# Optimization experiments

Measured on AMD Instinct MI355X. Metric: run time of the kernel, lower is better.

The kernel has to match this reference:

```python
import jax, jax.numpy as jnp
import numpy as np

E = 16      # num experts
K = 2       # top-k
EPS = np.finfo(float).eps


def setup_inputs() -> dict:
    key = jax.random.key(0)
    k1, k2, k3 = jax.random.split(key, 3)
    B, D_IN, D_OUT = 16384, 1024, 512
    x = jax.random.normal(k1, (B, D_IN), dtype=jnp.float32)
    w_router = jax.random.normal(k2, (D_IN, E), dtype=jnp.float32) * 0.02
    w_experts = jax.random.normal(k3, (E, D_IN, D_OUT), dtype=jnp.float32) * 0.02
    return {"x": x, "w_router": w_router, "w_experts": w_experts}


def reference(x, w_router, w_experts):
    # --- noisy_top_k_gating (eval path: clean logits, no noise) ---
    logits = x @ w_router                      # [B, E]
    top_vals, top_idx = jax.lax.top_k(logits, K)   # [B, K]
    top_gates = jax.nn.softmax(top_vals, axis=1)   # softmax over top-k logits
    B = x.shape[0]
    gates = jnp.zeros_like(logits).at[jnp.arange(B)[:, None], top_idx].set(top_gates)  # [B, E]

    # --- per-expert encode (dense form; zero gates null out non-dispatched pairs,
    #     matching SparseDispatcher's sparse dispatch/combine math exactly) ---
    expert_out = jnp.einsum('bd,edh->beh', x, w_experts)  # [B, E, d_out]

    # --- SparseDispatcher.combine: exp -> gate-weight -> index_add -> eps clamp -> log ---
    combined = jnp.einsum('be,beh->bh', gates, jnp.exp(expert_out))  # [B, d_out]
    combined = jnp.where(combined == 0, jnp.asarray(EPS, combined.dtype), combined)
    return jnp.log(combined)
```

## Files before the change

kernel.cpp:

```cpp
#include <hip/hip_runtime.h>
#include <hip/hip_bf16.h>

typedef unsigned short u16_t;
typedef unsigned int   u32_t;

#define B_ROWS  16384
#define D_IN    1024
#define D_OUT   512
#define NEXP    16
#define CNT_STRIDE 16
#define EPSF    2.2204460492503131e-16f

using short8  = __attribute__((ext_vector_type(8))) short;
using floatx4 = __attribute__((ext_vector_type(4))) float;

__device__ __forceinline__ u16_t f2bf(float f) {
    u32_t u = __float_as_uint(f);
    u += 0x7fffu + ((u >> 16) & 1u);
    return (u16_t)(u >> 16);
}

__global__ __launch_bounds__(256) void prep_kernel(
        const float* __restrict__ x, const float* __restrict__ wr,
        const float* __restrict__ we,
        u16_t* __restrict__ xb, float* __restrict__ wrT,
        u16_t* __restrict__ wT, int* __restrict__ counts) {
    __shared__ u16_t sh[128][72];
    int blk = blockIdx.x;
    int t = threadIdx.x;
    if (blk < 8192) {
        if (blk == 0) counts[t] = 0;
        size_t i = ((size_t)blk * 256 + t) * 8;
        float4 a = *(const float4*)(x + i);
        float4 b = *(const float4*)(x + i + 4);
        union { u16_t us[8]; uint4 v; } p;
        p.us[0] = f2bf(a.x); p.us[1] = f2bf(a.y); p.us[2] = f2bf(a.z); p.us[3] = f2bf(a.w);
        p.us[4] = f2bf(b.x); p.us[5] = f2bf(b.y); p.us[6] = f2bf(b.z); p.us[7] = f2bf(b.w);
        *(uint4*)(xb + i) = p.v;
    } else if (blk < 9216) {
        int b = blk - 8192;
        int e = b >> 6, k0 = ((b >> 3) & 7) * 128, n0 = (b & 7) * 64;
        int kk = t >> 4, nc = (t & 15) * 4;
        const float* src = we + ((size_t)e * D_IN + k0 + kk) * D_OUT + n0 + nc;
        #pragma unroll
        for (int p = 0; p < 8; ++p) {
            float4 v = *(const float4*)(src + (size_t)p * 16 * D_OUT);
            sh[p * 16 + kk][nc + 0] = f2bf(v.x);
            sh[p * 16 + kk][nc + 1] = f2bf(v.y);
            sh[p * 16 + kk][nc + 2] = f2bf(v.z);
            sh[p * 16 + kk][nc + 3] = f2bf(v.w);
        }
        __syncthreads();
        int nn = t >> 2, c = t & 3;
        u16_t* dst = wT + ((size_t)e * D_OUT + n0 + nn) * D_IN + k0 + c * 32;
        #pragma unroll
        for (int j = 0; j < 4; ++j) {
            union { u16_t us[8]; uint4 v; } p;
            #pragma unroll
            for (int jj = 0; jj < 8; ++jj) p.us[jj] = sh[c * 32 + j * 8 + jj][nn];
            *(uint4*)(dst + j * 8) = p.v;
        }
    } else {
        int i = (blk - 9216) * 256 + t;
        int e = i >> 10, d = i & 1023;
        wrT[i] = wr[d * NEXP + e];
    }
}

__global__ __launch_bounds__(256) void router_kernel(
        const float* __restrict__ x, const float* __restrict__ wrT,
        int* __restrict__ counts, int* __restrict__ rowlist,
        float* __restrict__ gatelist) {
    __shared__ float wsh[NEXP * D_IN];
    __shared__ int hist[NEXP], base[NEXP], hist2[NEXP];
    __shared__ unsigned char eidx_sh[32][2];
    __shared__ float g_sh[32][2];

    int t = threadIdx.x;
    {
        const float4* src = (const float4*)wrT;
        float4* dst = (float4*)wsh;
        #pragma unroll
        for (int i = 0; i < 16; ++i) dst[t + 256 * i] = src[t + 256 * i];
    }
    if (t < NEXP) { hist[t] = 0; hist2[t] = 0; }
    __syncthreads();

    int lr = t >> 3, q = t & 7;
    int row = blockIdx.x * 32 + lr;
    const float4* xq = (const float4*)(x + (size_t)row * D_IN);

    double acc[NEXP];
    #pragma unroll
    for (int e = 0; e < NEXP; ++e) acc[e] = 0.0;

    for (int i = 0; i < 32; ++i) {
        float4 xv = xq[i * 8 + q];
        double x0 = xv.x, x1 = xv.y, x2 = xv.z, x3 = xv.w;
        #pragma unroll
        for (int e = 0; e < NEXP; ++e) {
            float4 wv = *(const float4*)(&wsh[e * D_IN + i * 32 + q * 4]);
            acc[e] += x0 * (double)wv.x;
            acc[e] += x1 * (double)wv.y;
            acc[e] += x2 * (double)wv.z;
            acc[e] += x3 * (double)wv.w;
        }
    }
    #pragma unroll
    for (int e = 0; e < NEXP; ++e) {
        acc[e] += __shfl_xor(acc[e], 1);
        acc[e] += __shfl_xor(acc[e], 2);
        acc[e] += __shfl_xor(acc[e], 4);
    }
    if (q == 0) {
        int i1 = 0; double v1 = acc[0];
        #pragma unroll
        for (int e = 1; e < NEXP; ++e) if (acc[e] > v1) { v1 = acc[e]; i1 = e; }
        int i2 = -1; double v2 = -1.0e300;
        #pragma unroll
        for (int e = 0; e < NEXP; ++e) if (e != i1 && acc[e] > v2) { v2 = acc[e]; i2 = e; }
        double ed = exp(v2 - v1);
        double s = 1.0 + ed;
        eidx_sh[lr][0] = (unsigned char)i1; g_sh[lr][0] = (float)(1.0 / s);
        eidx_sh[lr][1] = (unsigned char)i2; g_sh[lr][1] = (float)(ed / s);
        atomicAdd(&hist[i1], 1);
        atomicAdd(&hist[i2], 1);
    }
    __syncthreads();
    if (t < NEXP) base[t] = atomicAdd(&counts[t * CNT_STRIDE], hist[t]);
    __syncthreads();
    if (t < 64) {
        int r = t >> 1, sl = t & 1;
        int e = eidx_sh[r][sl];
        int pos = base[e] + atomicAdd(&hist2[e], 1);
        rowlist[e * B_ROWS + pos] = ((blockIdx.x * 32 + r) << 1) | sl;
        gatelist[e * B_ROWS + pos] = g_sh[r][sl];
    }
}

template<bool USE_CONTRIB>
__global__ __launch_bounds__(256) void moe_gemm_bf16(
        const u16_t* __restrict__ xb, const u16_t* __restrict__ wT,
        const int* __restrict__ counts, const int* __restrict__ rowlist,
        const float* __restrict__ gatelist,
        float* __restrict__ out, float* __restrict__ contrib) {
    int e = blockIdx.z;
    int n_e = counts[e * CNT_STRIDE];
    int ty = blockIdx.y;
    if (ty * 128 >= n_e) return;
    int n0 = blockIdx.x * 128;

    __shared__ __align__(16) u16_t Af[4096];
    __shared__ __align__(16) u16_t Bf[4096];
    __shared__ int   rid_sh[128];
    __shared__ float gt_sh[128];

    int t = threadIdx.x;
    if (t < 128) {
        int gi = ty * 128 + t;
        int v = 0; float g = 0.f;
        if (gi < n_e) { v = rowlist[e * B_ROWS + gi]; g = gatelist[e * B_ROWS + gi]; }
        rid_sh[t] = v; gt_sh[t] = g;
    }
    __syncthreads();

    int s_lm = t & 15, s_q = (t >> 4) & 3, s_tile = t >> 6;
    int rowA0 = s_tile * 16 + s_lm, rowA1 = rowA0 + 64;
    const u16_t* aG0 = xb + (size_t)(rid_sh[rowA0] >> 1) * D_IN + s_q * 8;
    const u16_t* aG1 = xb + (size_t)(rid_sh[rowA1] >> 1) * D_IN + s_q * 8;
    const u16_t* bG0 = wT + ((size_t)e * D_OUT + n0 + rowA0) * D_IN + s_q * 8;
    const u16_t* bG1 = wT + ((size_t)e * D_OUT + n0 + rowA1) * D_IN + s_q * 8;
    u16_t* aL0 = Af + t * 8;
    u16_t* aL1 = Af + (t + 256) * 8;
    u16_t* bL0 = Bf + t * 8;
    u16_t* bL1 = Bf + (t + 256) * 8;

    int lane = t & 63, wv = t >> 6;
    int wm = wv >> 1, wn = wv & 1;
    int lm = lane & 15, q = lane >> 4;

    floatx4 acc[4][4];
    #pragma unroll
    for (int mi = 0; mi < 4; ++mi)
        #pragma unroll
        for (int ni = 0; ni < 4; ++ni)
            acc[mi][ni] = (floatx4){0.f, 0.f, 0.f, 0.f};

    for (int it = 0; it < D_IN / 32; ++it) {
        uint4 a0 = *(const uint4*)aG0;
        uint4 a1 = *(const uint4*)aG1;
        uint4 b0 = *(const uint4*)bG0;
        uint4 b1 = *(const uint4*)bG1;
        aG0 += 32; aG1 += 32; bG0 += 32; bG1 += 32;

        __syncthreads();
        *(uint4*)aL0 = a0;
        *(uint4*)aL1 = a1;
        *(uint4*)bL0 = b0;
        *(uint4*)bL1 = b1;
        __syncthreads();

        short8 afr[4], bfr[4];
        #pragma unroll
        for (int mi = 0; mi < 4; ++mi)
            afr[mi] = *(const short8*)(Af + ((wm * 4 + mi) * 64 + lane) * 8);
        #pragma unroll
        for (int ni = 0; ni < 4; ++ni)
            bfr[ni] = *(const short8*)(Bf + ((wn * 4 + ni) * 64 + lane) * 8);
        #pragma unroll
        for (int mi = 0; mi < 4; ++mi)
            #pragma unroll
            for (int ni = 0; ni < 4; ++ni)
                acc[mi][ni] = __builtin_amdgcn_mfma_f32_16x16x32_bf16(
                    afr[mi], bfr[ni], acc[mi][ni], 0, 0, 0);
    }

    #pragma unroll
    for (int mi = 0; mi < 4; ++mi) {
        int rbase = wm * 64 + mi * 16 + q * 4;
        #pragma unroll
        for (int r = 0; r < 4; ++r) {
            int row = rbase + r;
            int gi = ty * 128 + row;
            bool ok = gi < n_e;
            int v = rid_sh[row];
            float g = gt_sh[row];
            size_t orow = (size_t)(v >> 1) * D_OUT;
            #pragma unroll
            for (int ni = 0; ni < 4; ++ni) {
                int c = n0 + wn * 64 + ni * 16 + lm;
                float val = g * __expf(acc[mi][ni][r]);
                if (ok) {
                    if (USE_CONTRIB) {
                        float* dst = (v & 1) ? contrib : out;
                        dst[orow + c] = val;
                    } else {
                        atomicAdd(&out[orow + c], val);
                    }
                }
            }
        }
    }
}

template<bool USE_CONTRIB>
__global__ __launch_bounds__(256) void moe_gemm(
        const float* __restrict__ x, const float* __restrict__ w,
        const int* __restrict__ counts, const int* __restrict__ rowlist,
        const float* __restrict__ gatelist,
        float* __restrict__ out, float* __restrict__ contrib) {
    int e = blockIdx.z;
    int n_e = counts[e * CNT_STRIDE];
    int ty = blockIdx.y;
    if (ty * 128 >= n_e) return;
    int n0 = blockIdx.x * 128;

    __shared__ u16_t Ash[128][40];
    __shared__ u32_t Bsh[16][132];
    __shared__ int   rid_sh[128];
    __shared__ float gt_sh[128];

    int t = threadIdx.x;
    if (t < 128) {
        int gi = ty * 128 + t;
        int v = 0; float g = 0.f;
        if (gi < n_e) { v = rowlist[e * B_ROWS + gi]; g = gatelist[e * B_ROWS + gi]; }
        rid_sh[t] = v; gt_sh[t] = g;
    }
    __syncthreads();

    int ar = t >> 1, ah = t & 1;
    const float* xptr = x + (size_t)(rid_sh[ar] >> 1) * D_IN + ah * 16;
    int bkp = t >> 4, bng = t & 15;
    const float* wptr = w + (size_t)e * (D_IN * D_OUT)
                          + (size_t)(2 * bkp) * D_OUT + n0 + bng * 8;

    int lane = t & 63, wv = t >> 6;
    int wm = wv >> 1, wn = wv & 1;
    int lm = lane & 15, q = lane >> 4;

    floatx4 acc[4][4];
    #pragma unroll
    for (int mi = 0; mi < 4; ++mi)
        #pragma unroll
        for (int ni = 0; ni < 4; ++ni)
            acc[mi][ni] = (floatx4){0.f, 0.f, 0.f, 0.f};

    for (int it = 0; it < D_IN / 32; ++it) {
        float4 av0 = *(const float4*)(xptr + 0);
        float4 av1 = *(const float4*)(xptr + 4);
        float4 av2 = *(const float4*)(xptr + 8);
        float4 av3 = *(const float4*)(xptr + 12);
        xptr += 32;
        float4 b0 = *(const float4*)(wptr + 0);
        float4 b1 = *(const float4*)(wptr + 4);
        float4 b2 = *(const float4*)(wptr + D_OUT);
        float4 b3 = *(const float4*)(wptr + D_OUT + 4);
        wptr += 32 * D_OUT;

        __syncthreads();
        {
            union { u16_t us[16]; uint4 v[2]; } ap;
            float af[16] = {av0.x, av0.y, av0.z, av0.w, av1.x, av1.y, av1.z, av1.w,
                            av2.x, av2.y, av2.z, av2.w, av3.x, av3.y, av3.z, av3.w};
            #pragma unroll
            for (int j = 0; j < 16; ++j) ap.us[j] = f2bf(af[j]);
            *(uint4*)(&Ash[ar][ah * 16])     = ap.v[0];
            *(uint4*)(&Ash[ar][ah * 16 + 8]) = ap.v[1];
        }
        {
            union { u32_t up[8]; uint4 v[2]; } bp;
            bp.up[0] = (u32_t)f2bf(b0.x) | ((u32_t)f2bf(b2.x) << 16);
            bp.up[1] = (u32_t)f2bf(b0.y) | ((u32_t)f2bf(b2.y) << 16);
            bp.up[2] = (u32_t)f2bf(b0.z) | ((u32_t)f2bf(b2.z) << 16);
            bp.up[3] = (u32_t)f2bf(b0.w) | ((u32_t)f2bf(b2.w) << 16);
            bp.up[4] = (u32_t)f2bf(b1.x) | ((u32_t)f2bf(b3.x) << 16);
            bp.up[5] = (u32_t)f2bf(b1.y) | ((u32_t)f2bf(b3.y) << 16);
            bp.up[6] = (u32_t)f2bf(b1.z) | ((u32_t)f2bf(b3.z) << 16);
            bp.up[7] = (u32_t)f2bf(b1.w) | ((u32_t)f2bf(b3.w) << 16);
            *(uint4*)(&Bsh[bkp][bng * 8])     = bp.v[0];
            *(uint4*)(&Bsh[bkp][bng * 8 + 4]) = bp.v[1];
        }
        __syncthreads();

        short8 afr[4];
        #pragma unroll
        for (int mi = 0; mi < 4; ++mi)
            afr[mi] = *(const short8*)(&Ash[wm * 64 + mi * 16 + lm][q * 8]);
        short8 bfr[4];
        #pragma unroll
        for (int ni = 0; ni < 4; ++ni) {
            int nn = wn * 64 + ni * 16 + lm;
            union { uint4 u; short8 s; } cv;
            cv.u.x = Bsh[q * 4 + 0][nn];
            cv.u.y = Bsh[q * 4 + 1][nn];
            cv.u.z = Bsh[q * 4 + 2][nn];
            cv.u.w = Bsh[q * 4 + 3][nn];
            bfr[ni] = cv.s;
        }
        #pragma unroll
        for (int mi = 0; mi < 4; ++mi)
            #pragma unroll
            for (int ni = 0; ni < 4; ++ni)
                acc[mi][ni] = __builtin_amdgcn_mfma_f32_16x16x32_bf16(
                    afr[mi], bfr[ni], acc[mi][ni], 0, 0, 0);
    }

    #pragma unroll
    for (int mi = 0; mi < 4; ++mi) {
        int rbase = wm * 64 + mi * 16 + q * 4;
        #pragma unroll
        for (int r = 0; r < 4; ++r) {
            int row = rbase + r;
            int gi = ty * 128 + row;
            bool ok = gi < n_e;
            int v = rid_sh[row];
            float g = gt_sh[row];
            size_t orow = (size_t)(v >> 1) * D_OUT;
            #pragma unroll
            for (int ni = 0; ni < 4; ++ni) {
                int c = n0 + wn * 64 + ni * 16 + lm;
                float val = g * __expf(acc[mi][ni][r]);
                if (ok) {
                    if (USE_CONTRIB) {
                        float* dst = (v & 1) ? contrib : out;
                        dst[orow + c] = val;
                    } else {
                        atomicAdd(&out[orow + c], val);
                    }
                }
            }
        }
    }
}

__global__ __launch_bounds__(256) void combine_add_log(
        float* __restrict__ out, const float* __restrict__ contrib, int n4) {
    int i = blockIdx.x * blockDim.x + threadIdx.x;
    if (i >= n4) return;
    float4 a = ((const float4*)out)[i];
    float4 b = ((const float4*)contrib)[i];
    float4 r;
    float s;
    s = a.x + b.x; s = (s == 0.f) ? EPSF : s; r.x = __logf(s);
    s = a.y + b.y; s = (s == 0.f) ? EPSF : s; r.y = __logf(s);
    s = a.z + b.z; s = (s == 0.f) ? EPSF : s; r.z = __logf(s);
    s = a.w + b.w; s = (s == 0.f) ? EPSF : s; r.w = __logf(s);
    ((float4*)out)[i] = r;
}

__global__ __launch_bounds__(256) void log_inplace(float* __restrict__ out, int n4) {
    int i = blockIdx.x * blockDim.x + threadIdx.x;
    if (i >= n4) return;
    float4 a = ((float4*)out)[i];
    float4 r;
    float s;
    s = a.x; s = (s == 0.f) ? EPSF : s; r.x = __logf(s);
    s = a.y; s = (s == 0.f) ? EPSF : s; r.y = __logf(s);
    s = a.z; s = (s == 0.f) ? EPSF : s; r.z = __logf(s);
    s = a.w; s = (s == 0.f) ? EPSF : s; r.w = __logf(s);
    ((float4*)out)[i] = r;
}

extern "C" void kernel_launch(void* const* d_in, const int* in_sizes, int n_in,
                              void* d_out, int out_size, void* d_ws, size_t ws_size,
                              hipStream_t stream) {
    const float* x  = (const float*)d_in[0];
    const float* wr = (const float*)d_in[1];
    const float* we = (const float*)d_in[2];
    float* out = (float*)d_out;
    char* ws = (char*)d_ws;

    size_t off = 0;
    int*   counts  = (int*)(ws + off);   off += 1024;
    int*   rowlist = (int*)(ws + off);   off += (size_t)NEXP * B_ROWS * 4;
    float* gates   = (float*)(ws + off); off += (size_t)NEXP * B_ROWS * 4;
    float* wrT     = (float*)(ws + off); off += (size_t)NEXP * D_IN * 4;
    float* contrib = (float*)(ws + off); off += (size_t)B_ROWS * D_OUT * 4;
    size_t tier2_need = off;
    u16_t* xb      = (u16_t*)(ws + off); off += (size_t)B_ROWS * D_IN * 2;
    u16_t* wTb     = (u16_t*)(ws + off); off += (size_t)NEXP * D_IN * D_OUT * 2;
    size_t tier3_need = off;

    dim3 g(D_OUT / 128, B_ROWS / 128, NEXP);
    int n4 = B_ROWS * D_OUT / 4;

    if (ws_size >= tier3_need) {
        prep_kernel<<<9280, 256, 0, stream>>>(x, wr, we, xb, wrT, wTb, counts);
        router_kernel<<<B_ROWS / 32, 256, 0, stream>>>(x, wrT, counts, rowlist, gates);
        moe_gemm_bf16<true><<<g, 256, 0, stream>>>(xb, wTb, counts, rowlist, gates, out, contrib);
        combine_add_log<<<(n4 + 255) / 256, 256, 0, stream>>>(out, contrib, n4);
    } else if (ws_size >= tier2_need) {
        hipMemsetAsync(counts, 0, 1024, stream);
        transpose_wr_dummy: ;
        {
        }
        extern __global__ void transpose_wr_k(const float*, float*);
        transpose_wr_k<<<NEXP * D_IN / 256, 256, 0, stream>>>(wr, wrT);
        router_kernel<<<B_ROWS / 32, 256, 0, stream>>>(x, wrT, counts, rowlist, gates);
        moe_gemm<true><<<g, 256, 0, stream>>>(x, we, counts, rowlist, gates, out, contrib);
        combine_add_log<<<(n4 + 255) / 256, 256, 0, stream>>>(out, contrib, n4);
    } else {
        hipMemsetAsync(counts, 0, 1024, stream);
        extern __global__ void transpose_wr_k(const float*, float*);
        transpose_wr_k<<<NEXP * D_IN / 256, 256, 0, stream>>>(wr, wrT);
        router_kernel<<<B_ROWS / 32, 256, 0, stream>>>(x, wrT, counts, rowlist, gates);
        hipMemsetAsync(out, 0, (size_t)B_ROWS * D_OUT * 4, stream);
        moe_gemm<false><<<g, 256, 0, stream>>>(x, we, counts, rowlist, gates, out, nullptr);
        log_inplace<<<(n4 + 255) / 256, 256, 0, stream>>>(out, n4);
    }
}

__global__ __launch_bounds__(256) void transpose_wr_k(
        const float* __restrict__ wr, float* __restrict__ wrT) {
    int i = blockIdx.x * 256 + threadIdx.x;
    int e = i >> 10, d = i & 1023;
    wrT[i] = wr[d * NEXP + e];
}
```

Before: 279.4 us.

## Route in fp32 with fp64 fixup for near-ties; compact expert grid

The router now accumulates logits in fp32 instead of fp64. Rows whose top-3 logit gaps fall below a tolerance are flagged and recomputed in double precision by a small fixup kernel, so the expert selection still matches the reference. Separately, the GEMM grid changes from a 3D grid with one z-slice per expert, where many blocks exit early, to a flat list of y-blocks that a prefix scan over the expert counts maps to (expert, tile). This removes fp64 throughput cost and idle block launches, but adds an extra kernel launch, global atomics for flagged rows, and a fixed YBLOCKS bound that assumes enough blocks to cover all expert tiles.

```diff
diff --git a/kernel.cpp b/kernel.cpp
--- a/kernel.cpp
+++ b/kernel.cpp
@@ -10,6 +10,8 @@
 #define NEXP    16
 #define CNT_STRIDE 16
 #define EPSF    2.2204460492503131e-16f
+#define TAU     2.0e-3f
+#define YBLOCKS 272
 
 using short8  = __attribute__((ext_vector_type(8))) short;
 using floatx4 = __attribute__((ext_vector_type(4))) float;
@@ -24,12 +26,12 @@
         const float* __restrict__ x, const float* __restrict__ wr,
         const float* __restrict__ we,
         u16_t* __restrict__ xb, float* __restrict__ wrT,
-        u16_t* __restrict__ wT, int* __restrict__ counts) {
+        u16_t* __restrict__ wT, int* __restrict__ counts, int* __restrict__ hdr) {
     __shared__ u16_t sh[128][72];
     int blk = blockIdx.x;
     int t = threadIdx.x;
     if (blk < 8192) {
-        if (blk == 0) counts[t] = 0;
+        if (blk == 0) { counts[t] = 0; if (t < 64) hdr[t] = 0; }
         size_t i = ((size_t)blk * 256 + t) * 8;
         float4 a = *(const float4*)(x + i);
         float4 b = *(const float4*)(x + i + 4);
@@ -67,10 +69,11 @@
     }
 }
 
-__global__ __launch_bounds__(256) void router_kernel(
+__global__ __launch_bounds__(256) void router_f32(
         const float* __restrict__ x, const float* __restrict__ wrT,
         int* __restrict__ counts, int* __restrict__ rowlist,
-        float* __restrict__ gatelist) {
+        float* __restrict__ gatelist, int* __restrict__ hdr,
+        int* __restrict__ flagrows) {
     __shared__ float wsh[NEXP * D_IN];
     __shared__ int hist[NEXP], base[NEXP], hist2[NEXP];
     __shared__ unsigned char eidx_sh[32][2];
@@ -90,20 +93,19 @@
     int row = blockIdx.x * 32 + lr;
     const float4* xq = (const float4*)(x + (size_t)row * D_IN);
 
-    double acc[NEXP];
+    float acc[NEXP];
     #pragma unroll
-    for (int e = 0; e < NEXP; ++e) acc[e] = 0.0;
+    for (int e = 0; e < NEXP; ++e) acc[e] = 0.f;
 
     for (int i = 0; i < 32; ++i) {
         float4 xv = xq[i * 8 + q];
-        double x0 = xv.x, x1 = xv.y, x2 = xv.z, x3 = xv.w;
         #pragma unroll
         for (int e = 0; e < NEXP; ++e) {
             float4 wv = *(const float4*)(&wsh[e * D_IN + i * 32 + q * 4]);
-            acc[e] += x0 * (double)wv.x;
-            acc[e] += x1 * (double)wv.y;
-            acc[e] += x2 * (double)wv.z;
-            acc[e] += x3 * (double)wv.w;
+            acc[e] = fmaf(xv.x, wv.x, acc[e]);
+            acc[e] = fmaf(xv.y, wv.y, acc[e]);
+            acc[e] = fmaf(xv.z, wv.z, acc[e]);
+            acc[e] = fmaf(xv.w, wv.w, acc[e]);
         }
     }
     #pragma unroll
@@ -113,18 +115,27 @@
         acc[e] += __shfl_xor(acc[e], 4);
     }
     if (q == 0) {
-        int i1 = 0; double v1 = acc[0];
+        int i1 = 0; float v1 = acc[0];
         #pragma unroll
         for (int e = 1; e < NEXP; ++e) if (acc[e] > v1) { v1 = acc[e]; i1 = e; }
-        int i2 = -1; double v2 = -1.0e300;
+        int i2 = -1; float v2 = -3.0e38f;
         #pragma unroll
         for (int e = 0; e < NEXP; ++e) if (e != i1 && acc[e] > v2) { v2 = acc[e]; i2 = e; }
-        double ed = exp(v2 - v1);
-        double s = 1.0 + ed;
-        eidx_sh[lr][0] = (unsigned char)i1; g_sh[lr][0] = (float)(1.0 / s);
-        eidx_sh[lr][1] = (unsigned char)i2; g_sh[lr][1] = (float)(ed / s);
-        atomicAdd(&hist[i1], 1);
-        atomicAdd(&hist[i2], 1);
+        float v3 = -3.0e38f;
+        #pragma unroll
+        for (int e = 0; e < NEXP; ++e) if (e != i1 && e != i2 && acc[e] > v3) v3 = acc[e];
+        if ((v1 - v2 < TAU) || (v2 - v3 < TAU)) {
+            int p = atomicAdd(&hdr[0], 1);
+            flagrows[p] = row;
+            eidx_sh[lr][0] = 255; eidx_sh[lr][1] = 255;
+        } else {
+            float ed = __expf(v2 - v1);
+            float s = 1.f + ed;
+            eidx_sh[lr][0] = (unsigned char)i1; g_sh[lr][0] = 1.f / s;
+            eidx_sh[lr][1] = (unsigned char)i2; g_sh[lr][1] = ed / s;
+            atomicAdd(&hist[i1], 1);
+            atomicAdd(&hist[i2], 1);
+        }
     }
     __syncthreads();
     if (t < NEXP) base[t] = atomicAdd(&counts[t * CNT_STRIDE], hist[t]);
@@ -132,10 +143,64 @@
     if (t < 64) {
         int r = t >> 1, sl = t & 1;
         int e = eidx_sh[r][sl];
-        int pos = base[e] + atomicAdd(&hist2[e], 1);
-        rowlist[e * B_ROWS + pos] = ((blockIdx.x * 32 + r) << 1) | sl;
-        gatelist[e * B_ROWS + pos] = g_sh[r][sl];
-    }
+        if (e != 255) {
+            int pos = base[e] + atomicAdd(&hist2[e], 1);
+            rowlist[e * B_ROWS + pos] = ((blockIdx.x * 32 + r) << 1) | sl;
+            gatelist[e * B_ROWS + pos] = g_sh[r][sl];
+        }
+    }
+}
+
+__global__ __launch_bounds__(256) void router_fix(
+        const float* __restrict__ x, const float* __restrict__ wrT,
+        int* __restrict__ counts, int* __restrict__ rowlist,
+        float* __restrict__ gatelist, const int* __restrict__ hdr,
+        const int* __restrict__ flagrows) {
+    int t = threadIdx.x, wv = t >> 6, lane = t & 63;
+    int nflag = hdr[0];
+    int e = lane & 15, qq = lane >> 4;
+    for (int j = blockIdx.x * 4 + wv; j < nflag; j += 64) {
+        int row = flagrows[j];
+        const float* xr_ = x + (size_t)row * D_IN + qq * 256;
+        const float* wr_ = wrT + (size_t)e * D_IN + qq * 256;
+        double a0 = 0.0, a1 = 0.0;
+        for (int i = 0; i < 128; ++i) {
+            a0 += (double)xr_[2 * i]     * (double)wr_[2 * i];
+            a1 += (double)xr_[2 * i + 1] * (double)wr_[2 * i + 1];
+        }
+        double acc = a0 + a1;
+        acc += __shfl_xor(acc, 16);
+        acc += __shfl_xor(acc, 32);
+        int i1 = -1; double v1 = -1e300;
+        for (int ee = 0; ee < NEXP; ++ee) {
+            double tt = __shfl(acc, ee);
+            if (tt > v1) { v1 = tt; i1 = ee; }
+        }
+        int i2 = -1; double v2 = -1e300;
+        for (int ee = 0; ee < NEXP; ++ee) {
+            double tt = __shfl(acc, ee);
+            if (ee != i1 && tt > v2) { v2 = tt; i2 = ee; }
+        }
+        if (lane == 0) {
+            double ed = exp(v2 - v1), s = 1.0 + ed;
+            int p1 = atomicAdd(&counts[i1 * CNT_STRIDE], 1);
+            rowlist[i1 * B_ROWS + p1] = (row << 1);
+            gatelist[i1 * B_ROWS + p1] = (float)(1.0 / s);
+            int p2 = atomicAdd(&counts[i2 * CNT_STRIDE], 1);
+            rowlist[i2 * B_ROWS + p2] = (row << 1) | 1;
+            gatelist[i2 * B_ROWS + p2] = (float)(ed / s);
+        }
+    }
+}
+
+__device__ __forceinline__ int map_yblock(const int* counts, int yc, int* ty) {
+    int acc0 = 0;
+    for (int e2 = 0; e2 < NEXP; ++e2) {
+        int nb = (counts[e2 * CNT_STRIDE] + 127) >> 7;
+        if (yc < acc0 + nb) { *ty = yc - acc0; return e2; }
+        acc0 += nb;
+    }
+    return -1;
 }
 
 template<bool USE_CONTRIB>
@@ -144,10 +209,10 @@
         const int* __restrict__ counts, const int* __restrict__ rowlist,
         const float* __restrict__ gatelist,
         float* __restrict__ out, float* __restrict__ contrib) {
-    int e = blockIdx.z;
+    int ty;
+    int e = map_yblock(counts, blockIdx.y, &ty);
+    if (e < 0) return;
     int n_e = counts[e * CNT_STRIDE];
-    int ty = blockIdx.y;
-    if (ty * 128 >= n_e) return;
     int n0 = blockIdx.x * 128;
 
     __shared__ __align__(16) u16_t Af[4096];
@@ -249,10 +314,10 @@
         const int* __restrict__ counts, const int* __restrict__ rowlist,
         const float* __restrict__ gatelist,
         float* __restrict__ out, float* __restrict__ contrib) {
-    int e = blockIdx.z;
+    int ty;
+    int e = map_yblock(counts, blockIdx.y, &ty);
+    if (e < 0) return;
     int n_e = counts[e * CNT_STRIDE];
-    int ty = blockIdx.y;
-    if (ty * 128 >= n_e) return;
     int n0 = blockIdx.x * 128;
 
     __shared__ u16_t Ash[128][40];
@@ -402,6 +467,13 @@
     ((float4*)out)[i] = r;
 }
 
+__global__ __launch_bounds__(256) void transpose_wr_k(
+        const float* __restrict__ wr, float* __restrict__ wrT) {
+    int i = blockIdx.x * 256 + threadIdx.x;
+    int e = i >> 10, d = i & 1023;
+    wrT[i] = wr[d * NEXP + e];
+}
+
 extern "C" void kernel_launch(void* const* d_in, const int* in_sizes, int n_in,
                               void* d_out, int out_size, void* d_ws, size_t ws_size,
                               hipStream_t stream) {
@@ -412,48 +484,41 @@
     char* ws = (char*)d_ws;
 
     size_t off = 0;
-    int*   counts  = (int*)(ws + off);   off += 1024;
-    int*   rowlist = (int*)(ws + off);   off += (size_t)NEXP * B_ROWS * 4;
-    float* gates   = (float*)(ws + off); off += (size_t)NEXP * B_ROWS * 4;
-    float* wrT     = (float*)(ws + off); off += (size_t)NEXP * D_IN * 4;
-    float* contrib = (float*)(ws + off); off += (size_t)B_ROWS * D_OUT * 4;
+    int*   counts   = (int*)(ws + off);   off += 1024;
+    int*   hdr      = (int*)(ws + off);   off += 256;
+    int*   flagrows = (int*)(ws + off);   off += (size_t)B_ROWS * 4;
+    int*   rowlist  = (int*)(ws + off);   off += (size_t)NEXP * B_ROWS * 4;
+    float* gates    = (float*)(ws + off); off += (size_t)NEXP * B_ROWS * 4;
+    float* wrT      = (float*)(ws + off); off += (size_t)NEXP * D_IN * 4;
+    float* contrib  = (float*)(ws + off); off += (size_t)B_ROWS * D_OUT * 4;
     size_t tier2_need = off;
-    u16_t* xb      = (u16_t*)(ws + off); off += (size_t)B_ROWS * D_IN * 2;
-    u16_t* wTb     = (u16_t*)(ws + off); off += (size_t)NEXP * D_IN * D_OUT * 2;
+    u16_t* xb       = (u16_t*)(ws + off); off += (size_t)B_ROWS * D_IN * 2;
+    u16_t* wTb      = (u16_t*)(ws + off); off += (size_t)NEXP * D_IN * D_OUT * 2;
     size_t tier3_need = off;
 
-    dim3 g(D_OUT / 128, B_ROWS / 128, NEXP);
+    dim3 g(D_OUT / 128, YBLOCKS, 1);
     int n4 = B_ROWS * D_OUT / 4;
 
     if (ws_size >= tier3_need) {
-        prep_kernel<<<9280, 256, 0, stream>>>(x, wr, we, xb, wrT, wTb, counts);
-        router_kernel<<<B_ROWS / 32, 256, 0, stream>>>(x, wrT, counts, rowlist, gates);
+        prep_kernel<<<9280, 256, 0, stream>>>(x, wr, we, xb, wrT, wTb, counts, hdr);
+        router_f32<<<B_ROWS / 32, 256, 0, stream>>>(x, wrT, counts, rowlist, gates, hdr, flagrows);
+        router_fix<<<16, 256, 0, stream>>>(x, wrT, counts, rowlist, gates, hdr, flagrows);
         moe_gemm_bf16<true><<<g, 256, 0, stream>>>(xb, wTb, counts, rowlist, gates, out, contrib);
         combine_add_log<<<(n4 + 255) / 256, 256, 0, stream>>>(out, contrib, n4);
     } else if (ws_size >= tier2_need) {
-        hipMemsetAsync(counts, 0, 1024, stream);
-        transpose_wr_dummy: ;
-        {
-        }
-        extern __global__ void transpose_wr_k(const float*, float*);
+        hipMemsetAsync(counts, 0, 1280, stream);
         transpose_wr_k<<<NEXP * D_IN / 256, 256, 0, stream>>>(wr, wrT);
-        router_kernel<<<B_ROWS / 32, 256, 0, stream>>>(x, wrT, counts, rowlist, gates);
+        router_f32<<<B_ROWS / 32, 256, 0, stream>>>(x, wrT, counts, rowlist, gates, hdr, flagrows);
+        router_fix<<<16, 256, 0, stream>>>(x, wrT, counts, rowlist, gates, hdr, flagrows);
         moe_gemm<true><<<g, 256, 0, stream>>>(x, we, counts, rowlist, gates, out, contrib);
         combine_add_log<<<(n4 + 255) / 256, 256, 0, stream>>>(out, contrib, n4);
     } else {
-        hipMemsetAsync(counts, 0, 1024, stream);
-        extern __global__ void transpose_wr_k(const float*, float*);
+        hipMemsetAsync(counts, 0, 1280, stream);
         transpose_wr_k<<<NEXP * D_IN / 256, 256, 0, stream>>>(wr, wrT);
-        router_kernel<<<B_ROWS / 32, 256, 0, stream>>>(x, wrT, counts, rowlist, gates);
+        router_f32<<<B_ROWS / 32, 256, 0, stream>>>(x, wrT, counts, rowlist, gates, hdr, flagrows);
+        router_fix<<<16, 256, 0, stream>>>(x, wrT, counts, rowlist, gates, hdr, flagrows);
         hipMemsetAsync(out, 0, (size_t)B_ROWS * D_OUT * 4, stream);
         moe_gemm<false><<<g, 256, 0, stream>>>(x, we, counts, rowlist, gates, out, nullptr);
         log_inplace<<<(n4 + 255) / 256, 256, 0, stream>>>(out, n4);
     }
 }
-
-__global__ __launch_bounds__(256) void transpose_wr_k(
-        const float* __restrict__ wr, float* __restrict__ wrT) {
-    int i = blockIdx.x * 256 + threadIdx.x;
-    int e = i >> 10, d = i & 1023;
-    wrT[i] = wr[d * NEXP + e];
-}
```

Result: slower. 323.2 us (+15.7%).
